# Kernel tuning notes

Measured on AMD Instinct MI355X. Metric: run time of the kernel, lower is better.

The kernel has to match this reference:

```python
import jax, jax.numpy as jnp
import numpy as np

D = 1024
H = 8
HD = D // H
SCALE = HD ** -0.5


def setup_inputs() -> dict:
    key = jax.random.key(0)
    ks = jax.random.split(key, 12)
    s = 0.02
    return {
        "x": jax.random.normal(ks[0], (4, 2048, D), dtype=jnp.float32),
        "attn_mask": jax.random.randint(ks[1], (2048, 2048), 0, 2, dtype=jnp.int32),
        "qkv_w": jax.random.normal(ks[2], (3 * D, D), dtype=jnp.float32) * s,
        "qkv_b": jnp.zeros((3 * D,), dtype=jnp.float32),
        "q_w": jax.random.normal(ks[3], (D, D), dtype=jnp.float32) * s,
        "q_b": jnp.zeros((D,), dtype=jnp.float32),
        "k_w": jax.random.normal(ks[4], (D, D), dtype=jnp.float32) * s,
        "k_b": jnp.zeros((D,), dtype=jnp.float32),
        "v_w": jax.random.normal(ks[5], (D, D), dtype=jnp.float32) * s,
        "v_b": jnp.zeros((D,), dtype=jnp.float32),
        "out_w": jax.random.normal(ks[6], (D, D), dtype=jnp.float32) * s,
        "out_b": jnp.zeros((D,), dtype=jnp.float32),
    }


def reference(x, attn_mask, qkv_w, qkv_b, q_w, q_b, k_w, k_b, v_w, v_b, out_w, out_b):
    B, S, _ = x.shape
    qkv = x @ qkv_w.T + qkv_b
    q, k, v = jnp.split(qkv, 3, axis=-1)
    # per-stream multi-head projections, then split heads: [B,H,S,HD]
    def heads(t, w, b):
        return (t @ w.T + b).reshape(B, S, H, HD).transpose(0, 2, 1, 3)
    q = heads(q, q_w, q_b)
    k = heads(k, k_w, k_b)
    v = heads(v, v_w, v_b)
    # scaled dot-product attention with masked softmax
    scores = jnp.einsum("bhqd,bhkd->bhqk", q, k) * SCALE
    scores = jnp.where(attn_mask == 1, -jnp.inf, scores)
    attn = jax.nn.softmax(scores, axis=-1)
    o = jnp.einsum("bhqk,bhkd->bhqd", attn, v)
    o = o.transpose(0, 2, 1, 3).reshape(B, S, D)
    return o @ out_w.T + out_b
```

## Files before the change

kernel.cpp:

```cpp
#include <hip/hip_runtime.h>
#include <stdint.h>

typedef unsigned short u16;
typedef unsigned int u32;
typedef unsigned long long u64;
using f32x4 = __attribute__((ext_vector_type(4))) float;
using f32x16 = __attribute__((ext_vector_type(16))) float;
using s16x8 = __attribute__((ext_vector_type(8))) short;
using u16x4 = __attribute__((ext_vector_type(4))) unsigned short;
using u32x4 = __attribute__((ext_vector_type(4))) u32;

static constexpr float kQScale = (float)(0.08838834764831845 * 1.4426950408889634);

__device__ __forceinline__ u16 f2bf(float f) {
  uint32_t u = __float_as_uint(f);
  u += 0x7fffu + ((u >> 16) & 1u);
  return (u16)(u >> 16);
}

__device__ __forceinline__ float fexp2(float x) {
#if __has_builtin(__builtin_amdgcn_exp2f)
  return __builtin_amdgcn_exp2f(x);
#else
  return exp2f(x);
#endif
}

__device__ __forceinline__ u32 cvtpk(float lo, float hi) {
  u32 r;
  asm("v_cvt_pk_bf16_f32 %0, %1, %2" : "=v"(r) : "v"(lo), "v"(hi));
  return r;
}

__device__ __forceinline__ void mfma16(f32x4& d, s16x8 a, s16x8 b) {
  asm volatile("v_mfma_f32_16x16x32_bf16 %0, %1, %2, %0" : "+v"(d) : "v"(a), "v"(b));
}
__device__ __forceinline__ void mfma32(f32x16& d, s16x8 a, s16x8 b) {
  asm volatile("v_mfma_f32_32x32x16_bf16 %0, %1, %2, %0" : "+v"(d) : "v"(a), "v"(b));
}
__device__ __forceinline__ f32x16 mfma32_z(s16x8 a, s16x8 b) {
  f32x16 d;
  asm volatile("v_mfma_f32_32x32x16_bf16 %0, %1, %2, 0" : "=&v"(d) : "v"(a), "v"(b));
  return d;
}

__device__ __forceinline__ void g2lds16(const void* g, void* l) {
  __builtin_amdgcn_global_load_lds(
      (__attribute__((address_space(1))) void*)(uintptr_t)g,
      (__attribute__((address_space(3))) void*)(uint32_t)(uintptr_t)l, 16, 0, 0);
}

#define BAR() asm volatile("s_barrier" ::: "memory")

__global__ __launch_bounds__(256) void prep(const float* __restrict__ x, u16* __restrict__ xb,
                                            const float* __restrict__ qw, const float* __restrict__ kw,
                                            const float* __restrict__ vw, const float* __restrict__ ow,
                                            u16* __restrict__ wb4,
                                            const float* __restrict__ qkvw, u16* __restrict__ qkvwT,
                                            const float* __restrict__ qkvb, const float* __restrict__ qb,
                                            const float* __restrict__ kb, const float* __restrict__ vb,
                                            float* __restrict__ cb3,
                                            const int* __restrict__ am, u64* __restrict__ pm) {
  __shared__ u16 tile[32][33];
  const int bid = blockIdx.x, tid = threadIdx.x;
  if (bid < 8192) {
    int i = (bid * 256 + tid) * 4;
    f32x4 v = *(const f32x4*)(x + i);
    u16x4 o = {f2bf(v.x), f2bf(v.y), f2bf(v.z), f2bf(v.w)};
    *(u16x4*)(xb + i) = o;
  } else if (bid < 12288) {
    int idx = bid - 8192;
    int z = idx >> 10;
    const float* in = z == 0 ? qw : z == 1 ? kw : z == 2 ? vw : ow;
    int i = ((idx & 1023) * 256 + tid) * 4;
    f32x4 v = *(const f32x4*)(in + i);
    u16x4 o = {f2bf(v.x), f2bf(v.y), f2bf(v.z), f2bf(v.w)};
    *(u16x4*)(wb4 + (size_t)z * 1048576 + i) = o;
  } else if (bid < 15360) {
    int idx = bid - 12288;
    int bx = idx & 31, by = idx >> 5;
    int tx = tid & 31, ty = tid >> 5;
#pragma unroll
    for (int k = 0; k < 4; ++k)
      tile[ty + k * 8][tx] = f2bf(qkvw[(size_t)(by * 32 + ty + k * 8) * 1024 + bx * 32 + tx]);
    __syncthreads();
#pragma unroll
    for (int k = 0; k < 4; ++k)
      qkvwT[(size_t)(bx * 32 + ty + k * 8) * 3072 + by * 32 + tx] = tile[tx][ty + k * 8];
  } else if (bid < 16128) {
    int idx = bid - 15360;
    int z = idx >> 8;
    const float* w = z == 0 ? qw : (z == 1 ? kw : vw);
    const float* ba = z == 0 ? qb : (z == 1 ? kb : vb);
    const float* bi = qkvb + z * 1024;
    int o = (idx & 255) * 4 + (tid >> 6);
    int lane = tid & 63;
    float s = 0.f;
    for (int m = lane; m < 1024; m += 64) s += w[o * 1024 + m] * bi[m];
#pragma unroll
    for (int d = 1; d < 64; d <<= 1) s += __shfl_xor(s, d);
    if (lane == 0) {
      float fin = s + ba[o];
      if (z == 0) fin *= kQScale;
      cb3[z * 1024 + o] = fin;
    }
  } else {
    int row = bid - 16128;
    int wv = tid >> 6, lane = tid & 63;
#pragma unroll
    for (int i = 0; i < 8; ++i) {
      int word = wv * 8 + i;
      u64 b = __ballot(am[(size_t)row * 2048 + word * 64 + lane] == 0);
      if (lane == 0) pm[(size_t)row * 32 + word] = b;
    }
  }
}

template <typename OUT_T, bool BIAS_PER_ROW>
__global__ __launch_bounds__(256, 2) void gemm_nt(const u16* __restrict__ A, int lda, long bsA,
                                                  const u16* __restrict__ B, int ldb, long bsB,
                                                  OUT_T* __restrict__ C, int ldc, long bsC,
                                                  const float* __restrict__ bias, long bsBias,
                                                  int NtilesN, int K, float scale_z0) {
  __shared__ __align__(16) u16 As[128 * 64];
  __shared__ __align__(16) u16 Bs[128 * 64];
  const int z = blockIdx.z;
  const float sc = (z == 0) ? scale_z0 : 1.f;
  A += (size_t)z * bsA; B += (size_t)z * bsB; C += (size_t)z * bsC;
  if (bias) bias += (size_t)z * bsBias;
  const int tm = blockIdx.x / NtilesN, tn = blockIdx.x % NtilesN;
  const int tid = threadIdx.x, lane = tid & 63, w = tid >> 6;
  const int wm = w >> 1, wn = w & 1;
  const int q = lane & 15, g = lane >> 4;
  f32x4 acc[4][4] = {};

  const u16* Ab = A + (size_t)(tm * 128 + (tid >> 3)) * lda + ((tid & 7) << 3);
  const u16* Bb = B + (size_t)(tn * 128 + (tid >> 3)) * ldb + ((tid & 7) << 3);
  char* AsW = (char*)As + (w << 10);
  char* BsW = (char*)Bs + (w << 10);

  for (int k0 = 0; k0 < K; k0 += 64) {
#pragma unroll
    for (int it = 0; it < 4; ++it) {
      g2lds16(Ab + (size_t)(it * 32) * lda + k0, AsW + it * 4096);
      g2lds16(Bb + (size_t)(it * 32) * ldb + k0, BsW + it * 4096);
    }
    __syncthreads();
#pragma unroll
    for (int kk = 0; kk < 2; ++kk) {
      s16x8 af[4], bf[4];
#pragma unroll
      for (int i = 0; i < 4; ++i)
        af[i] = *(const s16x8*)((const char*)As + (wm * 64 + i * 16 + q) * 128 + kk * 64 + g * 16);
#pragma unroll
      for (int i = 0; i < 4; ++i)
        bf[i] = *(const s16x8*)((const char*)Bs + (wn * 64 + i * 16 + q) * 128 + kk * 64 + g * 16);
#pragma unroll
      for (int mf = 0; mf < 4; ++mf)
#pragma unroll
        for (int nf = 0; nf < 4; ++nf) mfma16(acc[mf][nf], af[mf], bf[nf]);
    }
    __syncthreads();
  }
  asm volatile("s_nop 7\n\ts_nop 7");
#pragma unroll
  for (int mf = 0; mf < 4; ++mf)
#pragma unroll
    for (int nf = 0; nf < 4; ++nf) {
      const int row = tm * 128 + wm * 64 + mf * 16 + g * 4;
      const int col = tn * 128 + wn * 64 + nf * 16 + q;
      float bc = (!BIAS_PER_ROW && bias) ? bias[col] : 0.f;
#pragma unroll
      for (int r = 0; r < 4; ++r) {
        float v = acc[mf][nf][r] * sc;
        if (bias) v += BIAS_PER_ROW ? bias[row + r] : bc;
        if constexpr (sizeof(OUT_T) == 2)
          C[(size_t)(row + r) * ldc + col] = (OUT_T)f2bf(v);
        else
          C[(size_t)(row + r) * ldc + col] = (OUT_T)v;
      }
    }
}

__global__ __launch_bounds__(512, 1) void gemm256_qkv(const u16* __restrict__ xb,
                                                      const u16* __restrict__ comb3,
                                                      const float* __restrict__ cb3,
                                                      u16* __restrict__ QK2,
                                                      u16* __restrict__ V2t) {
  __shared__ __align__(16) u16 Als[2][256 * 64];
  __shared__ __align__(16) u16 Bls[2][256 * 64];
  const int bid = blockIdx.x;
  const int cpx = gridDim.x >> 3;
  const int wgid = (bid & 7) * cpx + (bid >> 3);
  const bool isV = wgid >= 256;
  const u16 *A, *B;
  u16* C;
  const float* bias;
  int lda, ldb, ldc, tm, tn;
  if (!isV) {
    tm = wgid >> 3; tn = wgid & 7;
    A = xb; lda = 1024; B = comb3; ldb = 1024; C = QK2; ldc = 2048; bias = cb3;
  } else {
    int id = wgid - 256;
    tm = id >> 5; tn = id & 31;
    A = comb3 + 2 * 1048576; lda = 1024; B = xb; ldb = 1024; C = V2t; ldc = 8192;
    bias = cb3 + 2048;
  }
  const int tid = threadIdx.x, lane = tid & 63, w = tid >> 6;
  const int wm = w >> 2, wn = w & 3;
  const int q = lane & 15, g = lane >> 4, qk = q & 7;
  const int nT = 16;

  f32x4 acc[8][4] = {};
  s16x8 af[4][2], bf[4][2];

  const int srow = tid >> 3, sch = tid & 7;
  const int gcol = (sch ^ (srow & 7)) << 3;
  const u16* Abase = A + (size_t)(tm * 256 + srow) * lda + gcol;
  const u16* Bbase = B + (size_t)(tn * 256 + srow) * ldb + gcol;

  auto stageA = [&](int buf, int kt, int h) {
    const u16* s0 = Abase + (size_t)(h * 128) * lda + (kt << 6);
    char* d = (char*)&Als[buf][0] + h * 16384 + (w << 10);
    g2lds16(s0, d);
    g2lds16(s0 + (size_t)64 * lda, d + 8192);
  };
  auto stageB = [&](int buf, int kt, int h) {
    const u16* s0 = Bbase + (size_t)(h * 128) * ldb + (kt << 6);
    char* d = (char*)&Bls[buf][0] + h * 16384 + (w << 10);
    g2lds16(s0, d);
    g2lds16(s0 + (size_t)64 * ldb, d + 8192);
  };
  auto loadA = [&](const char* base, int mh) {
#pragma unroll
    for (int mf = 0; mf < 4; ++mf)
#pragma unroll
      for (int kk = 0; kk < 2; ++kk)
        af[mf][kk] = *(const s16x8*)(base + (mh * 128 + wm * 64 + mf * 16 + q) * 128 +
                                     ((((kk << 2) + g) ^ qk) << 4));
  };
  auto loadB = [&](const char* base, int nh) {
#pragma unroll
    for (int nf = 0; nf < 2; ++nf)
#pragma unroll
      for (int kk = 0; kk < 2; ++kk)
        bf[nh * 2 + nf][kk] = *(const s16x8*)(base + (nh * 128 + wn * 32 + nf * 16 + q) * 128 +
                                              ((((kk << 2) + g) ^ qk) << 4));
  };
  auto quad = [&](int mh, int nh) {
    __builtin_amdgcn_s_setprio(1);
#pragma unroll
    for (int mf = 0; mf < 4; ++mf)
#pragma unroll
      for (int nf = 0; nf < 2; ++nf)
#pragma unroll
        for (int kk = 0; kk < 2; ++kk)
          mfma16(acc[mh * 4 + mf][nh * 2 + nf], af[mf][kk], bf[nh * 2 + nf][kk]);
    __builtin_amdgcn_s_setprio(0);
  };

  stageA(0, 0, 0); stageA(0, 0, 1); stageB(0, 0, 0); stageB(0, 0, 1);
  stageB(1, 1, 0); stageB(1, 1, 1);
  asm volatile("s_waitcnt vmcnt(4)" ::: "memory");
  BAR();

  for (int kt = 0; kt < nT; ++kt) {
    const int buf = kt & 1;
    const char* Ab = (const char*)&Als[buf][0];
    const char* Bb = (const char*)&Bls[buf][0];
    const int ktA = (kt + 1 < nT) ? kt + 1 : nT - 1;
    const int ktB = (kt + 2 < nT) ? kt + 2 : nT - 1;
    loadA(Ab, 0); loadB(Bb, 0);
    stageA(buf ^ 1, ktA, 0);
    BAR();
    quad(0, 0);
    BAR();
    loadB(Bb, 1);
    stageA(buf ^ 1, ktA, 1);
    BAR();
    quad(0, 1);
    asm volatile("s_waitcnt vmcnt(8)" ::: "memory");
    BAR();
    loadA(Ab, 1);
    stageB(buf, ktB, 0);
    BAR();
    quad(1, 0);
    BAR();
    stageB(buf, ktB, 1);
    BAR();
    quad(1, 1);
    asm volatile("s_waitcnt vmcnt(6)" ::: "memory");
    BAR();
  }

  asm volatile("s_nop 7\n\ts_nop 7");
#pragma unroll
  for (int mf = 0; mf < 8; ++mf) {
    const int row = tm * 256 + (mf >> 2) * 128 + wm * 64 + (mf & 3) * 16 + g * 4;
#pragma unroll
    for (int nf = 0; nf < 4; ++nf) {
      const int col = tn * 256 + (nf >> 1) * 128 + wn * 32 + (nf & 1) * 16 + q;
      const float bc = isV ? 0.f : bias[col];
#pragma unroll
      for (int r = 0; r < 4; ++r) {
        float v = acc[mf][nf][r] + (isV ? bias[row + r] : bc);
        C[(size_t)(row + r) * ldc + col] = f2bf(v);
      }
    }
  }
}

__global__ __launch_bounds__(256, 2) void attn_fwd(const u16* __restrict__ Qb, const u16* __restrict__ Kb,
                                                   int ldq, const u16* __restrict__ Vt,
                                                   const u64* __restrict__ pmask,
                                                   u16* __restrict__ Ob) {
  __shared__ __align__(16) char K_lds[2][16384];
  __shared__ __align__(16) char V_lds[3][16384];
  const int n = blockIdx.x;
  const int slot = n >> 3;
  const int grp = (n & 7) * 4 + (slot >> 4);
  const int qt = slot & 15;
  const int h = grp & 7, b = grp >> 3;
  const int tid = threadIdx.x, w = tid >> 6, lane = tid & 63;
  const int ql = lane & 31;
  const int hi = lane >> 5;
  const int q0 = qt * 128;

  s16x8 qf[8];
  const u16* qrow = Qb + (size_t)(b * 2048 + q0 + w * 32 + ql) * ldq + h * 128 + 8 * hi;
#pragma unroll
  for (int kd = 0; kd < 8; ++kd) qf[kd] = *(const s16x8*)(qrow + 16 * kd);

  u32x4 ov = {0x3F803F80u, 0x3F803F80u, 0x3F803F80u, 0x3F803F80u};
  const s16x8 ones = __builtin_bit_cast(s16x8, ov);

  f32x16 oacc[4] = {};
  f32x16 lacc = {};

  const int ksr = tid >> 4, ksc = tid & 15;
  const int vsr = tid >> 3, vsc = tid & 7;
  const int sw = ql & 15;
  const u64* pmrow = pmask + (size_t)(q0 + w * 32 + ql) * 32;

  auto stageK = [&](int buf, int s2) {
    const int kv0 = s2 * 64;
    char* kb = K_lds[buf] + (w << 10);
#pragma unroll
    for (int it = 0; it < 4; ++it) {
      int kr = it * 16 + ksr;
      g2lds16(Kb + (size_t)(b * 2048 + kv0 + kr) * ldq + h * 128 + ((ksc ^ (kr & 15)) << 3),
              kb + it * 4096);
    }
  };
  auto stageV = [&](int buf, int s2) {
    const int kv0 = s2 * 64;
    char* vb = V_lds[buf] + (w << 10);
#pragma unroll
    for (int it = 0; it < 4; ++it) {
      int vr = it * 32 + vsr;
      g2lds16(Vt + (size_t)(h * 128 + vr) * 8192 + b * 2048 + kv0 + ((vsc ^ (vr & 7)) << 3),
              vb + it * 4096);
    }
  };
  auto qk = [&](f32x16& d0, f32x16& d1, int kbuf) {
    const char* Kc = K_lds[kbuf];
#pragma unroll
    for (int kd = 0; kd < 8; ++kd) {
      int c = (2 * kd + hi) ^ sw;
      s16x8 kf0 = *(const s16x8*)(Kc + ql * 256 + (c << 4));
      s16x8 kf1 = *(const s16x8*)(Kc + (32 + ql) * 256 + (c << 4));
      if (kd == 0) { d0 = mfma32_z(kf0, qf[0]); d1 = mfma32_z(kf1, qf[0]); }
      else         { mfma32(d0, kf0, qf[kd]);   mfma32(d1, kf1, qf[kd]); }
    }
  };

  auto body = [&](f32x16& c0, f32x16& c1, f32x16& n0, f32x16& n1, int s, int vbR, int vbW) {
    u64 pw = pmrow[s];
    const int sc2 = (s + 2 < 32) ? s + 2 : 31;
    stageK(s & 1, sc2);
    stageV(vbW, sc2);
    if (s + 1 < 32) qk(n0, n1, (s + 1) & 1);
    const char* Vc = V_lds[vbR];
    s16x8 pa[2];
#pragma unroll
    for (int half = 0; half < 2; ++half) {
      u32 halfm = (u32)(pw >> (32 * half + 4 * hi));
      u32 Wp[4][2];
#pragma unroll
      for (int t = 0; t < 4; ++t) {
        float e[4];
#pragma unroll
        for (int j = 0; j < 4; ++j) {
          float ev = fexp2(half == 0 ? c0[4 * t + j] : c1[4 * t + j]);
          int km;
          asm("v_bfe_i32 %0, %1, %2, 1" : "=v"(km) : "v"(halfm), "n"(8 * t + j));
          e[j] = __uint_as_float(__float_as_uint(ev) & (u32)km);
        }
        Wp[t][0] = cvtpk(e[0], e[1]);
        Wp[t][1] = cvtpk(e[2], e[3]);
      }
#pragma unroll
      for (int kq = 0; kq < 2; ++kq) {
        u32 s0 = hi ? Wp[2 * kq][0] : Wp[2 * kq + 1][0];
        u32 s1 = hi ? Wp[2 * kq][1] : Wp[2 * kq + 1][1];
        u32 r0 = (u32)__shfl_xor((int)s0, 32);
        u32 r1 = (u32)__shfl_xor((int)s1, 32);
        u32 o0 = hi ? Wp[2 * kq + 1][0] : Wp[2 * kq][0];
        u32 o1 = hi ? Wp[2 * kq + 1][1] : Wp[2 * kq][1];
        u32x4 wv;
        wv.x = hi ? r0 : o0;
        wv.y = hi ? r1 : o1;
        wv.z = hi ? o0 : r0;
        wv.w = hi ? o1 : r1;
        pa[kq] = __builtin_bit_cast(s16x8, wv);
      }
      asm volatile("s_nop 3");
      __builtin_amdgcn_s_setprio(1);
#pragma unroll
      for (int kq = 0; kq < 2; ++kq) {
        const int ks = 2 * half + kq;
#pragma unroll
        for (int dt = 0; dt < 4; ++dt) {
          int vrow = dt * 32 + ql;
          s16x8 vf = *(const s16x8*)(Vc + vrow * 128 + (((2 * ks + hi) ^ (vrow & 7)) << 4));
          mfma32(oacc[dt], pa[kq], vf);
        }
        mfma32(lacc, pa[kq], ones);
      }
      __builtin_amdgcn_s_setprio(0);
    }
    asm volatile("s_waitcnt vmcnt(4)" ::: "memory");
    BAR();
  };

  stageK(0, 0); stageV(0, 0); stageK(1, 1); stageV(1, 1);
  asm volatile("s_waitcnt vmcnt(4)" ::: "memory");
  BAR();
  f32x16 sA0, sA1, sB0, sB1;
  qk(sA0, sA1, 0);
  BAR();

  int vb = 0;
  for (int s2 = 0; s2 < 16; ++s2) {
    const int s = 2 * s2;
    const int vb1 = (vb + 1 == 3) ? 0 : vb + 1;
    const int vb2 = (vb + 2 >= 3) ? vb - 1 : vb + 2;
    body(sA0, sA1, sB0, sB1, s, vb, vb2);
    body(sB0, sB1, sA0, sA1, s + 1, vb1, vb);
    vb = vb2;
  }

  asm volatile("s_nop 7\n\ts_nop 7");
#pragma unroll
  for (int dt = 0; dt < 4; ++dt)
#pragma unroll
    for (int reg = 0; reg < 16; ++reg) {
      int qr = (reg & 3) + 8 * (reg >> 2) + 4 * hi;
      size_t trow = (size_t)(b * 2048 + q0 + w * 32 + qr);
      Ob[trow * 1024 + h * 128 + dt * 32 + ql] = f2bf(oacc[dt][reg] / lacc[reg]);
    }
}

extern "C" void kernel_launch(void* const* d_in, const int* in_sizes, int n_in,
                              void* d_out, int out_size, void* d_ws, size_t ws_size,
                              hipStream_t stream) {
  (void)in_sizes; (void)n_in; (void)out_size; (void)ws_size;
  const float* x    = (const float*)d_in[0];
  const int*   am   = (const int*)d_in[1];
  const float* qkvw = (const float*)d_in[2];
  const float* qkvb = (const float*)d_in[3];
  const float* qw   = (const float*)d_in[4];
  const float* qb   = (const float*)d_in[5];
  const float* kw   = (const float*)d_in[6];
  const float* kb   = (const float*)d_in[7];
  const float* vw   = (const float*)d_in[8];
  const float* vb   = (const float*)d_in[9];
  const float* ow   = (const float*)d_in[10];
  const float* ob   = (const float*)d_in[11];

  char* p = (char*)d_ws;
  auto take = [&](size_t n) { char* r = p; p += (n + 255) & ~(size_t)255; return r; };
  u16* xb    = (u16*)take(8192ull * 1024 * 2);
  u16* qkvwT = (u16*)take(1024ull * 3072 * 2);
  u16* wb4   = (u16*)take(4ull * 1048576 * 2);
  u16* comb3 = (u16*)take(3ull * 1048576 * 2);
  float* cb3 = (float*)take(3ull * 1024 * 4);
  u16* QK2   = (u16*)take(8192ull * 2048 * 2);
  u16* V2t   = (u16*)take(8192ull * 1024 * 2);
  u64* pm    = (u64*)take(2048ull * 32 * 8);
  u16* Obuf  = xb;

  prep<<<18176, 256, 0, stream>>>(x, xb, qw, kw, vw, ow, wb4, qkvw, qkvwT,
                                  qkvb, qb, kb, vb, cb3, am, pm);
  gemm_nt<u16, false><<<dim3(64, 1, 3), 256, 0, stream>>>(
      wb4, 1024, 1048576, qkvwT, 3072, 1024, comb3, 1024, 1048576, nullptr, 0, 8, 1024, kQScale);
  gemm256_qkv<<<384, 512, 0, stream>>>(xb, comb3, cb3, QK2, V2t);
  attn_fwd<<<512, 256, 0, stream>>>(QK2, QK2 + 1024, 2048, V2t, pm, Obuf);
  gemm_nt<float, false><<<dim3(512, 1, 1), 256, 0, stream>>>(
      Obuf, 1024, 0, wb4 + 3 * 1048576, 1024, 0, (float*)d_out, 1024, 0, ob, 0, 8, 1024, 1.f);
}
```

Before: 258.0 us.

## Split fused QKV GEMM into simpler single-buffered QK GEMM and separate V GEMM

Replaces the hand-pipelined 256x256 double-buffered fused Q/K/V GEMM with a simpler 256x128-tile QK GEMM that uses single-buffered LDS and a plain sync loop. The launch bounds now ask for 4 blocks per CU. The transposed V projection moves to the generic gemm_nt kernel with row bias, as a separate launch. The aim is higher occupancy and more blocks per GEMM, in exchange for losing the explicit load/compute overlap and adding one kernel launch.

```diff
diff --git a/kernel.cpp b/kernel.cpp
--- a/kernel.cpp
+++ b/kernel.cpp
@@ -182,130 +182,66 @@
     }
 }
 
-__global__ __launch_bounds__(512, 1) void gemm256_qkv(const u16* __restrict__ xb,
-                                                      const u16* __restrict__ comb3,
-                                                      const float* __restrict__ cb3,
-                                                      u16* __restrict__ QK2,
-                                                      u16* __restrict__ V2t) {
-  __shared__ __align__(16) u16 Als[2][256 * 64];
-  __shared__ __align__(16) u16 Bls[2][256 * 64];
+__global__ __launch_bounds__(512, 4) void gemm_qk(const u16* __restrict__ A,
+                                                  const u16* __restrict__ B,
+                                                  const float* __restrict__ bias,
+                                                  u16* __restrict__ C) {
+  __shared__ __align__(16) u16 As[256 * 64];
+  __shared__ __align__(16) u16 Bs[128 * 64];
   const int bid = blockIdx.x;
-  const int cpx = gridDim.x >> 3;
-  const int wgid = (bid & 7) * cpx + (bid >> 3);
-  const bool isV = wgid >= 256;
-  const u16 *A, *B;
-  u16* C;
-  const float* bias;
-  int lda, ldb, ldc, tm, tn;
-  if (!isV) {
-    tm = wgid >> 3; tn = wgid & 7;
-    A = xb; lda = 1024; B = comb3; ldb = 1024; C = QK2; ldc = 2048; bias = cb3;
-  } else {
-    int id = wgid - 256;
-    tm = id >> 5; tn = id & 31;
-    A = comb3 + 2 * 1048576; lda = 1024; B = xb; ldb = 1024; C = V2t; ldc = 8192;
-    bias = cb3 + 2048;
-  }
+  const int wgid = (bid & 7) * 64 + (bid >> 3);
+  const int tm = wgid >> 4, tn = wgid & 15;
   const int tid = threadIdx.x, lane = tid & 63, w = tid >> 6;
-  const int wm = w >> 2, wn = w & 3;
+  const int wm = w >> 1, wn = w & 1;
   const int q = lane & 15, g = lane >> 4, qk = q & 7;
-  const int nT = 16;
-
-  f32x4 acc[8][4] = {};
-  s16x8 af[4][2], bf[4][2];
+  f32x4 acc[4][4] = {};
 
   const int srow = tid >> 3, sch = tid & 7;
   const int gcol = (sch ^ (srow & 7)) << 3;
-  const u16* Abase = A + (size_t)(tm * 256 + srow) * lda + gcol;
-  const u16* Bbase = B + (size_t)(tn * 256 + srow) * ldb + gcol;
-
-  auto stageA = [&](int buf, int kt, int h) {
-    const u16* s0 = Abase + (size_t)(h * 128) * lda + (kt << 6);
-    char* d = (char*)&Als[buf][0] + h * 16384 + (w << 10);
-    g2lds16(s0, d);
-    g2lds16(s0 + (size_t)64 * lda, d + 8192);
-  };
-  auto stageB = [&](int buf, int kt, int h) {
-    const u16* s0 = Bbase + (size_t)(h * 128) * ldb + (kt << 6);
-    char* d = (char*)&Bls[buf][0] + h * 16384 + (w << 10);
-    g2lds16(s0, d);
-    g2lds16(s0 + (size_t)64 * ldb, d + 8192);
-  };
-  auto loadA = [&](const char* base, int mh) {
-#pragma unroll
-    for (int mf = 0; mf < 4; ++mf)
-#pragma unroll
-      for (int kk = 0; kk < 2; ++kk)
-        af[mf][kk] = *(const s16x8*)(base + (mh * 128 + wm * 64 + mf * 16 + q) * 128 +
-                                     ((((kk << 2) + g) ^ qk) << 4));
-  };
-  auto loadB = [&](const char* base, int nh) {
-#pragma unroll
-    for (int nf = 0; nf < 2; ++nf)
-#pragma unroll
-      for (int kk = 0; kk < 2; ++kk)
-        bf[nh * 2 + nf][kk] = *(const s16x8*)(base + (nh * 128 + wn * 32 + nf * 16 + q) * 128 +
-                                              ((((kk << 2) + g) ^ qk) << 4));
-  };
-  auto quad = [&](int mh, int nh) {
-    __builtin_amdgcn_s_setprio(1);
-#pragma unroll
-    for (int mf = 0; mf < 4; ++mf)
-#pragma unroll
-      for (int nf = 0; nf < 2; ++nf)
-#pragma unroll
-        for (int kk = 0; kk < 2; ++kk)
-          mfma16(acc[mh * 4 + mf][nh * 2 + nf], af[mf][kk], bf[nh * 2 + nf][kk]);
-    __builtin_amdgcn_s_setprio(0);
-  };
-
-  stageA(0, 0, 0); stageA(0, 0, 1); stageB(0, 0, 0); stageB(0, 0, 1);
-  stageB(1, 1, 0); stageB(1, 1, 1);
-  asm volatile("s_waitcnt vmcnt(4)" ::: "memory");
-  BAR();
-
-  for (int kt = 0; kt < nT; ++kt) {
-    const int buf = kt & 1;
-    const char* Ab = (const char*)&Als[buf][0];
-    const char* Bb = (const char*)&Bls[buf][0];
-    const int ktA = (kt + 1 < nT) ? kt + 1 : nT - 1;
-    const int ktB = (kt + 2 < nT) ? kt + 2 : nT - 1;
-    loadA(Ab, 0); loadB(Bb, 0);
-    stageA(buf ^ 1, ktA, 0);
-    BAR();
-    quad(0, 0);
-    BAR();
-    loadB(Bb, 1);
-    stageA(buf ^ 1, ktA, 1);
-    BAR();
-    quad(0, 1);
-    asm volatile("s_waitcnt vmcnt(8)" ::: "memory");
-    BAR();
-    loadA(Ab, 1);
-    stageB(buf, ktB, 0);
-    BAR();
-    quad(1, 0);
-    BAR();
-    stageB(buf, ktB, 1);
-    BAR();
-    quad(1, 1);
-    asm volatile("s_waitcnt vmcnt(6)" ::: "memory");
-    BAR();
+  const u16* Abase = A + (size_t)(tm * 256 + srow) * 1024 + gcol;
+  const u16* Bbase = B + (size_t)(tn * 128 + srow) * 1024 + gcol;
+  char* AsW = (char*)As + (w << 10);
+  char* BsW = (char*)Bs + (w << 10);
+
+  for (int k0 = 0; k0 < 1024; k0 += 64) {
+#pragma unroll
+    for (int it = 0; it < 4; ++it)
+      g2lds16(Abase + (size_t)(it * 64) * 1024 + k0, AsW + it * 8192);
+#pragma unroll
+    for (int it = 0; it < 2; ++it)
+      g2lds16(Bbase + (size_t)(it * 64) * 1024 + k0, BsW + it * 8192);
+    __syncthreads();
+#pragma unroll
+    for (int kk = 0; kk < 2; ++kk) {
+      s16x8 af[4], bf[4];
+#pragma unroll
+      for (int i = 0; i < 4; ++i)
+        af[i] = *(const s16x8*)((const char*)As + (wm * 64 + i * 16 + q) * 128 +
+                                ((((kk << 2) + g) ^ qk) << 4));
+#pragma unroll
+      for (int i = 0; i < 4; ++i)
+        bf[i] = *(const s16x8*)((const char*)Bs + (wn * 64 + i * 16 + q) * 128 +
+                                ((((kk << 2) + g) ^ qk) << 4));
+      __builtin_amdgcn_s_setprio(1);
+#pragma unroll
+      for (int mf = 0; mf < 4; ++mf)
+#pragma unroll
+        for (int nf = 0; nf < 4; ++nf) mfma16(acc[mf][nf], af[mf], bf[nf]);
+      __builtin_amdgcn_s_setprio(0);
+    }
+    __syncthreads();
   }
-
   asm volatile("s_nop 7\n\ts_nop 7");
 #pragma unroll
-  for (int mf = 0; mf < 8; ++mf) {
-    const int row = tm * 256 + (mf >> 2) * 128 + wm * 64 + (mf & 3) * 16 + g * 4;
+  for (int mf = 0; mf < 4; ++mf) {
+    const int row = tm * 256 + wm * 64 + mf * 16 + g * 4;
 #pragma unroll
     for (int nf = 0; nf < 4; ++nf) {
-      const int col = tn * 256 + (nf >> 1) * 128 + wn * 32 + (nf & 1) * 16 + q;
-      const float bc = isV ? 0.f : bias[col];
-#pragma unroll
-      for (int r = 0; r < 4; ++r) {
-        float v = acc[mf][nf][r] + (isV ? bias[row + r] : bc);
-        C[(size_t)(row + r) * ldc + col] = f2bf(v);
-      }
+      const int col = tn * 128 + wn * 64 + nf * 16 + q;
+      const float bc = bias[col];
+#pragma unroll
+      for (int r = 0; r < 4; ++r)
+        C[(size_t)(row + r) * 2048 + col] = f2bf(acc[mf][nf][r] + bc);
     }
   }
 }
@@ -494,7 +430,9 @@
                                   qkvb, qb, kb, vb, cb3, am, pm);
   gemm_nt<u16, false><<<dim3(64, 1, 3), 256, 0, stream>>>(
       wb4, 1024, 1048576, qkvwT, 3072, 1024, comb3, 1024, 1048576, nullptr, 0, 8, 1024, kQScale);
-  gemm256_qkv<<<384, 512, 0, stream>>>(xb, comb3, cb3, QK2, V2t);
+  gemm_qk<<<512, 512, 0, stream>>>(xb, comb3, cb3, QK2);
+  gemm_nt<u16, true><<<dim3(512, 1, 1), 256, 0, stream>>>(
+      comb3 + 2 * 1048576, 1024, 0, xb, 1024, 0, V2t, 8192, 0, cb3 + 2048, 0, 64, 1024, 1.f);
   attn_fwd<<<512, 256, 0, stream>>>(QK2, QK2 + 1024, 2048, V2t, pm, Obuf);
   gemm_nt<float, false><<<dim3(512, 1, 1), 256, 0, stream>>>(
       Obuf, 1024, 0, wb4 + 3 * 1048576, 1024, 0, (float*)d_out, 1024, 0, ob, 0, 8, 1024, 1.f);
```

Result: faster. 239.3 us (-7.3%).
